# Kernel optimization log

Measured on AMD Instinct MI355X. Metric: run time of the kernel, lower is better.

## Reference

```python
import jax, jax.numpy as jnp
import numpy as np
import math

B, S, D_MODEL = 8, 1024, 1024
N_INPUT, N_PROCESS = 256, 512
N_HEADS, N_HEADS_IN = 8, 4
HIDDEN = 2 * N_INPUT  # combination_analyzer hidden dim (default n_input*2)
TEMP = 2.0            # router temperature buffer


def _mha(x, w_in, b_in, w_out, b_out, n_heads):
    """torch nn.MultiheadAttention (batch_first, eval mode) self-attention."""
    Bq, Sq, E = x.shape
    qkv = x @ w_in.T + b_in                      # [B,S,3E]
    q, k, v = jnp.split(qkv, 3, axis=-1)
    dh = E // n_heads
    sh = lambda t: t.reshape(Bq, Sq, n_heads, dh).transpose(0, 2, 1, 3)
    q, k, v = sh(q), sh(k), sh(v)
    scores = jnp.einsum('bhqd,bhkd->bhqk', q, k) * (1.0 / math.sqrt(dh))
    attn = jax.nn.softmax(scores, axis=-1)
    out = jnp.einsum('bhqk,bhkd->bhqd', attn, v).transpose(0, 2, 1, 3).reshape(Bq, Sq, E)
    return out @ w_out.T + b_out


def _ln(x, g, b, eps=1e-5):
    m = x.mean(-1, keepdims=True)
    v = ((x - m) ** 2).mean(-1, keepdims=True)
    return (x - m) / jnp.sqrt(v + eps) * g + b


def setup_inputs() -> dict:
    key = jax.random.key(0)
    ks = jax.random.split(key, 24)
    rn = lambda i, shape, s=0.02: jax.random.normal(ks[i], shape, jnp.float32) * s
    return {
        'x': jax.random.normal(ks[0], (B, S, D_MODEL), jnp.float32),
        # DynamicRouter attention (embed=d_model, heads=8)
        'r_in_w': rn(1, (3 * D_MODEL, D_MODEL)), 'r_in_b': jnp.zeros((3 * D_MODEL,), jnp.float32),
        'r_out_w': rn(2, (D_MODEL, D_MODEL)), 'r_out_b': jnp.zeros((D_MODEL,), jnp.float32),
        'aff_w': rn(3, (N_INPUT, D_MODEL)), 'aff_b': jnp.zeros((N_INPUT,), jnp.float32),
        # InputNeurons
        'patterns': rn(4, (N_INPUT, D_MODEL), 0.05),
        'i_in_w': rn(5, (3 * N_INPUT, N_INPUT)), 'i_in_b': jnp.zeros((3 * N_INPUT,), jnp.float32),
        'i_out_w': rn(6, (N_INPUT, N_INPUT)), 'i_out_b': jnp.zeros((N_INPUT,), jnp.float32),
        'ln_g': jnp.ones((N_INPUT,), jnp.float32), 'ln_b': jnp.zeros((N_INPUT,), jnp.float32),
        # ProcessNeurons
        'comb_w': rn(7, (N_PROCESS, N_INPUT), 0.05),
        'out_proj_w': rn(8, (N_PROCESS, D_MODEL), 0.05),
        'a1_w': rn(9, (HIDDEN, N_INPUT)), 'a1_b': jnp.zeros((HIDDEN,), jnp.float32),
        'a2_w': rn(10, (N_PROCESS, HIDDEN)), 'a2_b': jnp.zeros((N_PROCESS,), jnp.float32),
        'k_input': 128, 'k_process': 256,
    }


def reference(x, r_in_w, r_in_b, r_out_w, r_out_b, aff_w, aff_b, patterns,
              i_in_w, i_in_b, i_out_w, i_out_b, ln_g, ln_b,
              comb_w, out_proj_w, a1_w, a1_b, a2_w, a2_b, k_input, k_process):
    Bq = x.shape[0]
    # ---- DynamicRouter (eval mode: no gumbel noise, no score noise) ----
    context = _mha(x, r_in_w, r_in_b, r_out_w, r_out_b, N_HEADS)      # [B,S,D]
    affinity = context @ aff_w.T + aff_b                              # [B,S,N_INPUT]
    scores = affinity.max(axis=1)                                     # [B,N_INPUT]
    logits = scores / TEMP
    soft_w = jax.nn.softmax(logits, axis=-1)
    _, indices = jax.lax.top_k(logits, k_input)                       # [B,k_in]
    mask = jnp.zeros_like(soft_w).at[jnp.arange(Bq)[:, None], indices].set(1.0)
    masked = soft_w * mask
    weights = masked / (masked.sum(-1, keepdims=True) + 1e-8)         # [B,N_INPUT]
    # ---- InputNeurons (eval: dropout off) ----
    acts = jax.nn.gelu(context @ patterns.T, approximate=False)       # [B,S,N_INPUT]
    attn_out = _mha(acts, i_in_w, i_in_b, i_out_w, i_out_b, N_HEADS_IN)
    acts = _ln(acts + attn_out, ln_g, ln_b)
    # ---- Gather routed input neurons, weighted by routing weights ----
    sel_acts = jnp.take_along_axis(acts, indices[:, None, :], axis=2)  # [B,S,k_in]
    sel_w = jnp.take_along_axis(weights, indices, axis=1)              # [B,k_in]
    sel_acts = sel_acts * sel_w[:, None, :]
    # ---- ProcessNeurons ----
    # selected_weights[b,p,j] = comb_w[p, indices[b,j]]
    sel_cw = jnp.take(comb_w, indices, axis=1).transpose(1, 0, 2)      # [B,P,k_in]
    proc_acts = jax.nn.gelu(jnp.einsum('bsk,bpk->bsp', sel_acts, sel_cw), approximate=False)
    input_sel = jnp.zeros((Bq, N_INPUT), jnp.float32).at[jnp.arange(Bq)[:, None], indices].set(1.0)
    relevance = jax.nn.gelu(input_sel @ a1_w.T + a1_b, approximate=False) @ a2_w.T + a2_b  # [B,P]
    act_scores = proc_acts.max(axis=1)                                 # [B,P]
    final_scores = act_scores * jax.nn.sigmoid(relevance)
    _, pidx = jax.lax.top_k(final_scores, k_process)                   # [B,k_p]
    sel_proc = jnp.take_along_axis(proc_acts, pidx[:, None, :], axis=2)  # [B,S,k_p]
    sel_proj = out_proj_w[pidx]                                        # [B,k_p,D]
    out = jnp.einsum('bsk,bkd->bsd', sel_proc, sel_proj)               # [B,S,D]
    # ---- residual (eval: dropout identity) ----
    return x + out
```

## Files before the change

### kernel.cpp

```cpp
#include <hip/hip_runtime.h>
#include <hip/hip_bf16.h>
#include <math.h>

constexpr int NB = 8, NS = 1024, ND = 1024, NIN = 256, NPROC = 512, KIN = 128, KPROC = 256;

typedef __attribute__((ext_vector_type(8))) short bf16x8;
typedef __attribute__((ext_vector_type(4))) float f32x4;

#define VMCNT(n) asm volatile("s_waitcnt vmcnt(" #n ")" ::: "memory")
#define LGKMCNT(n) asm volatile("s_waitcnt lgkmcnt(" #n ")" ::: "memory")

__device__ inline float gelu_f(float x) {
    return 0.5f * x * (1.0f + erff(x * 0.7071067811865476f));
}
__device__ inline unsigned short f2b(float f) {
    __hip_bfloat16 h = __float2bfloat16(f);
    return *reinterpret_cast<unsigned short*>(&h);
}
__device__ inline void gload16(const void* g, void* l) {
    __builtin_amdgcn_global_load_lds(
        (const __attribute__((address_space(1))) void*)g,
        (__attribute__((address_space(3))) void*)l, 16, 0, 0);
}

__global__ __launch_bounds__(256)
void cvt_all_kernel(const float* __restrict__ x, const float* __restrict__ rin,
                    const float* __restrict__ rout, const float* __restrict__ affw,
                    const float* __restrict__ patt, const float* __restrict__ iin,
                    const float* __restrict__ iout, const float* __restrict__ aff_b,
                    unsigned short* __restrict__ xb, unsigned short* __restrict__ rinb,
                    unsigned short* __restrict__ routb, unsigned short* __restrict__ affbw,
                    unsigned short* __restrict__ pattb, unsigned short* __restrict__ iinb,
                    unsigned short* __restrict__ ioutb, float* __restrict__ biascat)
{
    if (blockIdx.x == 0) {
        int t = threadIdx.x;
        biascat[t] = aff_b[t];
        biascat[256 + t] = 0.f;
    }
    long gi = (long)blockIdx.x * 256 + threadIdx.x;
    long stride = (long)gridDim.x * 256;
    for (; gi < 3342336; gi += stride) {
        const float4* s; ushort4* d; long off;
        if (gi < 2097152)      { s = (const float4*)x;    d = (ushort4*)xb;    off = gi; }
        else if (gi < 2883584) { s = (const float4*)rin;  d = (ushort4*)rinb;  off = gi - 2097152; }
        else if (gi < 3145728) { s = (const float4*)rout; d = (ushort4*)routb; off = gi - 2883584; }
        else if (gi < 3211264) { s = (const float4*)affw; d = (ushort4*)affbw; off = gi - 3145728; }
        else if (gi < 3276800) { s = (const float4*)patt; d = (ushort4*)pattb; off = gi - 3211264; }
        else if (gi < 3325952) { s = (const float4*)iin;  d = (ushort4*)iinb;  off = gi - 3276800; }
        else                   { s = (const float4*)iout; d = (ushort4*)ioutb; off = gi - 3325952; }
        float4 v = s[off];
        ushort4 o;
        o.x = f2b(v.x); o.y = f2b(v.y); o.z = f2b(v.z); o.w = f2b(v.w);
        d[off] = o;
    }
}

__global__ __launch_bounds__(256)
void gemm128s(const unsigned short* __restrict__ A, int lda,
              const unsigned short* __restrict__ B, int ldb,
              const float* __restrict__ bias,
              unsigned short* __restrict__ C16, int ldc,
              int K, int nbx)
{
    __shared__ __align__(16) unsigned short Ab[3][128 * 32];
    __shared__ __align__(16) unsigned short Bb[3][128 * 32];
    int o = blockIdx.x;
    int cpx = gridDim.x >> 3;
    int swz = (o & 7) * cpx + (o >> 3);
    int by = swz / nbx, bx = swz - by * nbx;
    int row0 = by * 128, col0 = bx * 128;

    int t = threadIdx.x;
    int w = t >> 6, l = t & 63, l15 = l & 15, g = l >> 4;
    int wr = w >> 1, wc = w & 1;
    int NT = K >> 5;

    f32x4 acc[4][4];
#pragma unroll
    for (int i = 0; i < 4; ++i)
#pragma unroll
        for (int j = 0; j < 4; ++j) acc[i][j] = (f32x4){0.f, 0.f, 0.f, 0.f};

    auto STAGE = [&](int c, int kt) {
        int k0 = kt * 32;
#pragma unroll
        for (int i = 0; i < 2; ++i) {
            int gi = t + i * 256;
            int row = gi >> 2, cg = gi & 3;
            int cgs = cg ^ ((row >> 1) & 3);
            gload16(&A[(long)(row0 + row) * lda + k0 + cgs * 8], &Ab[c][gi * 8]);
        }
#pragma unroll
        for (int i = 0; i < 2; ++i) {
            int gi = t + i * 256;
            int row = gi >> 2, cg = gi & 3;
            int cgs = cg ^ ((row >> 1) & 3);
            gload16(&B[(long)(col0 + row) * ldb + k0 + cgs * 8], &Bb[c][gi * 8]);
        }
    };

    STAGE(0, 0);
    STAGE(1, 1);

    int cbr = (g ^ ((l15 >> 1) & 3)) * 16;

    int cur = 0;
    for (int T = 0; T < NT; ++T) {
        if (T + 1 < NT) { VMCNT(4); } else { VMCNT(0); }
        __builtin_amdgcn_s_barrier();
        asm volatile("" ::: "memory");

        const char* Ab_ = (const char*)&Ab[cur][0];
        const char* Bb_ = (const char*)&Bb[cur][0];
        bf16x8 af[4], bfr[4];
#pragma unroll
        for (int mi = 0; mi < 4; ++mi)
            af[mi] = *(const bf16x8*)(Ab_ + (wr * 64 + mi * 16 + l15) * 64 + cbr);
#pragma unroll
        for (int ni = 0; ni < 4; ++ni)
            bfr[ni] = *(const bf16x8*)(Bb_ + (wc * 64 + ni * 16 + l15) * 64 + cbr);

        if (T + 2 < NT) {
            int nxt = cur + 2;
            if (nxt >= 3) nxt -= 3;
            STAGE(nxt, T + 2);
        }

        LGKMCNT(0);
        __builtin_amdgcn_sched_barrier(0);
        __builtin_amdgcn_s_setprio(1);
#pragma unroll
        for (int mi = 0; mi < 4; ++mi)
#pragma unroll
            for (int ni = 0; ni < 4; ++ni)
                acc[mi][ni] = __builtin_amdgcn_mfma_f32_16x16x32_bf16(
                    af[mi], bfr[ni], acc[mi][ni], 0, 0, 0);
        __builtin_amdgcn_s_setprio(0);

        cur = (cur == 2) ? 0 : cur + 1;
    }

#pragma unroll
    for (int mi = 0; mi < 4; ++mi) {
#pragma unroll
        for (int ni = 0; ni < 4; ++ni) {
            int col = col0 + wc * 64 + ni * 16 + l15;
            float bv = bias ? bias[col] : 0.f;
#pragma unroll
            for (int r = 0; r < 4; ++r) {
                int row = row0 + wr * 64 + mi * 16 + g * 4 + r;
                float v = acc[mi][ni][r] + bv;
                float vp = __shfl_xor(v, 1);
                if (!(l15 & 1)) {
                    unsigned int u = (unsigned int)f2b(v) | ((unsigned int)f2b(vp) << 16);
                    *(unsigned int*)&C16[(long)row * ldc + col] = u;
                }
            }
        }
    }
}

__global__ __launch_bounds__(256)
void gemm128x64(const unsigned short* __restrict__ A, int lda,
                const unsigned short* __restrict__ B, int ldb,
                const float* __restrict__ bias,
                unsigned short* __restrict__ C16, int ldc,
                int K, int nbx)
{
    __shared__ __align__(16) unsigned short Ab[3][128 * 32];
    __shared__ __align__(16) unsigned short Bb[3][64 * 32];
    int o = blockIdx.x;
    int cpx = gridDim.x >> 3;
    int swz = (o & 7) * cpx + (o >> 3);
    int by = swz / nbx, bx = swz - by * nbx;
    int row0 = by * 128, col0 = bx * 64;

    int t = threadIdx.x;
    int w = t >> 6, l = t & 63, l15 = l & 15, g = l >> 4;
    int wr = w >> 1, wc = w & 1;
    int NT = K >> 5;

    f32x4 acc[4][2];
#pragma unroll
    for (int i = 0; i < 4; ++i)
#pragma unroll
        for (int j = 0; j < 2; ++j) acc[i][j] = (f32x4){0.f, 0.f, 0.f, 0.f};

    auto STAGE = [&](int c, int kt) {
        int k0 = kt * 32;
#pragma unroll
        for (int i = 0; i < 2; ++i) {
            int gi = t + i * 256;
            int row = gi >> 2, cg = gi & 3;
            int cgs = cg ^ ((row >> 1) & 3);
            gload16(&A[(long)(row0 + row) * lda + k0 + cgs * 8], &Ab[c][gi * 8]);
        }
        {
            int gi = t;
            int row = gi >> 2, cg = gi & 3;
            int cgs = cg ^ ((row >> 1) & 3);
            gload16(&B[(long)(col0 + row) * ldb + k0 + cgs * 8], &Bb[c][gi * 8]);
        }
    };

    STAGE(0, 0);
    STAGE(1, 1);

    int cbr = (g ^ ((l15 >> 1) & 3)) * 16;

    int cur = 0;
    for (int T = 0; T < NT; ++T) {
        if (T + 1 < NT) { VMCNT(3); } else { VMCNT(0); }
        __builtin_amdgcn_s_barrier();
        asm volatile("" ::: "memory");

        const char* Ab_ = (const char*)&Ab[cur][0];
        const char* Bb_ = (const char*)&Bb[cur][0];
        bf16x8 af[4], bfr[2];
#pragma unroll
        for (int mi = 0; mi < 4; ++mi)
            af[mi] = *(const bf16x8*)(Ab_ + (wr * 64 + mi * 16 + l15) * 64 + cbr);
#pragma unroll
        for (int ni = 0; ni < 2; ++ni)
            bfr[ni] = *(const bf16x8*)(Bb_ + (wc * 32 + ni * 16 + l15) * 64 + cbr);

        if (T + 2 < NT) {
            int nxt = cur + 2;
            if (nxt >= 3) nxt -= 3;
            STAGE(nxt, T + 2);
        }

        LGKMCNT(0);
        __builtin_amdgcn_sched_barrier(0);
        __builtin_amdgcn_s_setprio(1);
#pragma unroll
        for (int mi = 0; mi < 4; ++mi)
#pragma unroll
            for (int ni = 0; ni < 2; ++ni)
                acc[mi][ni] = __builtin_amdgcn_mfma_f32_16x16x32_bf16(
                    af[mi], bfr[ni], acc[mi][ni], 0, 0, 0);
        __builtin_amdgcn_s_setprio(0);

        cur = (cur == 2) ? 0 : cur + 1;
    }

#pragma unroll
    for (int mi = 0; mi < 4; ++mi) {
#pragma unroll
        for (int ni = 0; ni < 2; ++ni) {
            int col = col0 + wc * 32 + ni * 16 + l15;
            float bv = bias ? bias[col] : 0.f;
#pragma unroll
            for (int r = 0; r < 4; ++r) {
                int row = row0 + wr * 64 + mi * 16 + g * 4 + r;
                float v = acc[mi][ni][r] + bv;
                float vp = __shfl_xor(v, 1);
                if (!(l15 & 1)) {
                    unsigned int u = (unsigned int)f2b(v) | ((unsigned int)f2b(vp) << 16);
                    *(unsigned int*)&C16[(long)row * ldc + col] = u;
                }
            }
        }
    }
}

__global__ __launch_bounds__(256)
void gemm128e(const unsigned short* __restrict__ A, long sA, int lda,
              const unsigned short* __restrict__ B, long sB, int ldb,
              const float* __restrict__ bias,
              const float* __restrict__ resid, long sR, int ldr,
              float* __restrict__ C32, long sC32, int ldc32,
              unsigned short* __restrict__ C16, long sC16, int ldc16,
              float* __restrict__ C32b, int ldc32b,
              int K, int nbx, int act)
{
    __shared__ __align__(16) unsigned short Ab[3][128 * 32];
    __shared__ __align__(16) unsigned short Bb[3][64 * 32];
    int bz = blockIdx.z;
    const unsigned short* Abase = A + (long)bz * sA;
    const unsigned short* Bbase = B + (long)bz * sB;
    int o = blockIdx.x;
    int cpx = gridDim.x >> 3;
    int swz = (o & 7) * cpx + (o >> 3);
    int by = swz / nbx, bx = swz - by * nbx;
    int row0 = by * 128, col0 = bx * 64;

    int t = threadIdx.x;
    int w = t >> 6, l = t & 63, l15 = l & 15, g = l >> 4;
    int wr = w >> 1, wc = w & 1;
    int NT = K >> 5;

    f32x4 acc[4][2];
#pragma unroll
    for (int i = 0; i < 4; ++i)
#pragma unroll
        for (int j = 0; j < 2; ++j) acc[i][j] = (f32x4){0.f, 0.f, 0.f, 0.f};

    auto STAGE = [&](int c, int kt) {
        int k0 = kt * 32;
#pragma unroll
        for (int i = 0; i < 2; ++i) {
            int gi = t + i * 256;
            int row = gi >> 2, cg = gi & 3;
            int cgs = cg ^ ((row >> 1) & 3);
            gload16(&Abase[(long)(row0 + row) * lda + k0 + cgs * 8], &Ab[c][gi * 8]);
        }
        {
            int gi = t;
            int row = gi >> 2, cg = gi & 3;
            int cgs = cg ^ ((row >> 1) & 3);
            gload16(&Bbase[(long)(col0 + row) * ldb + k0 + cgs * 8], &Bb[c][gi * 8]);
        }
    };

    STAGE(0, 0);
    STAGE(1, 1);

    int cbr = (g ^ ((l15 >> 1) & 3)) * 16;

    int cur = 0;
    for (int T = 0; T < NT; ++T) {
        if (T + 1 < NT) { VMCNT(3); } else { VMCNT(0); }
        __builtin_amdgcn_s_barrier();
        asm volatile("" ::: "memory");

        const char* Ab_ = (const char*)&Ab[cur][0];
        const char* Bb_ = (const char*)&Bb[cur][0];
        bf16x8 af[4], bfr[2];
#pragma unroll
        for (int mi = 0; mi < 4; ++mi)
            af[mi] = *(const bf16x8*)(Ab_ + (wr * 64 + mi * 16 + l15) * 64 + cbr);
#pragma unroll
        for (int ni = 0; ni < 2; ++ni)
            bfr[ni] = *(const bf16x8*)(Bb_ + (wc * 32 + ni * 16 + l15) * 64 + cbr);

        if (T + 2 < NT) {
            int nxt = cur + 2;
            if (nxt >= 3) nxt -= 3;
            STAGE(nxt, T + 2);
        }

        LGKMCNT(0);
        __builtin_amdgcn_sched_barrier(0);
        __builtin_amdgcn_s_setprio(1);
#pragma unroll
        for (int mi = 0; mi < 4; ++mi)
#pragma unroll
            for (int ni = 0; ni < 2; ++ni)
                acc[mi][ni] = __builtin_amdgcn_mfma_f32_16x16x32_bf16(
                    af[mi], bfr[ni], acc[mi][ni], 0, 0, 0);
        __builtin_amdgcn_s_setprio(0);

        cur = (cur == 2) ? 0 : cur + 1;
    }

#pragma unroll
    for (int mi = 0; mi < 4; ++mi) {
#pragma unroll
        for (int ni = 0; ni < 2; ++ni) {
            int col = col0 + wc * 32 + ni * 16 + l15;
            float bv = bias ? bias[col] : 0.f;
#pragma unroll
            for (int r = 0; r < 4; ++r) {
                int row = row0 + wr * 64 + mi * 16 + g * 4 + r;
                float v = acc[mi][ni][r] + bv;
                if (act == 2) {
                    if (col < 256) {
                        C32[(long)row * ldc32 + col] = v;
                    } else {
                        v = gelu_f(v);
                        C32b[(long)row * ldc32b + (col - 256)] = v;
                        C16[(long)row * ldc16 + (col - 256)] = f2b(v);
                    }
                    continue;
                }
                if (act == 1) v = gelu_f(v);
                if (resid) v += resid[(long)bz * sR + (long)row * ldr + col];
                if (C32) C32[(long)bz * sC32 + (long)row * ldc32 + col] = v;
                if (C16) C16[(long)bz * sC16 + (long)row * ldc16 + col] = f2b(v);
            }
        }
    }
}

template <int D>
__global__ __launch_bounds__(256, 2)
void attn_mfma(unsigned short* __restrict__ qkv, int stride, int koff, int voff, float scale)
{
    constexpr int GRL = D / 8;
    constexpr int NITK = (64 * GRL) / 256;
    constexpr int NITV = NITK;
    constexpr int NKS = D / 32;
    constexpr int NF = D / 16;
    constexpr int LV = 72;
    constexpr int LP = 72;
    constexpr int NT = NS / 64;

    __shared__ __align__(16) unsigned short Ks[2][64 * D];
    __shared__ __align__(16) unsigned short Vt[D * LV];
    __shared__ __align__(16) unsigned short Ps[128 * LP];

    int b = blockIdx.z, h = blockIdx.y, qt = blockIdx.x;
    int t = threadIdx.x, w = t >> 6, l = t & 63, l15 = l & 15, g = l >> 4;
    int wq = w * 32;
    long qbase = ((long)b * NS + qt * 128) * stride + h * D;
    long kvbase = (long)b * NS * stride + h * D;

    bf16x8 qreg[2][NKS];
#pragma unroll
    for (int qh = 0; qh < 2; ++qh)
#pragma unroll
        for (int ks = 0; ks < NKS; ++ks)
            qreg[qh][ks] = *(const bf16x8*)&qkv[qbase + (long)(wq + qh * 16 + l15) * stride + g * 8 + ks * 32];

    auto KSTAGE = [&](int c, int kt) {
#pragma unroll
        for (int i = 0; i < NITK; ++i) {
            int gi = t + i * 256;
            int row = gi / GRL, cg = gi % GRL;
            int cgs = cg ^ (row & 7);
            gload16(&qkv[kvbase + (long)(kt * 64 + row) * stride + koff + cgs * 8],
                    &Ks[c][gi * 8]);
        }
    };
    uint4 vp[NITV];
    auto VLOAD = [&](int kt) {
#pragma unroll
        for (int i = 0; i < NITV; ++i) {
            int vgi = t + i * 256;
            int kc = vgi & 63, db = vgi >> 6;
            vp[i] = *(const uint4*)&qkv[kvbase + (long)(kt * 64 + kc) * stride + voff + db * 8];
        }
    };
    auto VWRITE = [&]() {
#pragma unroll
        for (int i = 0; i < NITV; ++i) {
            int vgi = t + i * 256;
            int kc = vgi & 63, db = vgi >> 6;
            uint4 v = vp[i];
            Vt[(db * 8 + 0) * LV + kc] = (unsigned short)(v.x & 0xffff);
            Vt[(db * 8 + 1) * LV + kc] = (unsigned short)(v.x >> 16);
            Vt[(db * 8 + 2) * LV + kc] = (unsigned short)(v.y & 0xffff);
            Vt[(db * 8 + 3) * LV + kc] = (unsigned short)(v.y >> 16);
            Vt[(db * 8 + 4) * LV + kc] = (unsigned short)(v.z & 0xffff);
            Vt[(db * 8 + 5) * LV + kc] = (unsigned short)(v.z >> 16);
            Vt[(db * 8 + 6) * LV + kc] = (unsigned short)(v.w & 0xffff);
            Vt[(db * 8 + 7) * LV + kc] = (unsigned short)(v.w >> 16);
        }
    };

    KSTAGE(0, 0);
    VLOAD(0);
    KSTAGE(1, 1);
    if constexpr (NITK == 4) { VMCNT(4); } else { VMCNT(2); }
    VWRITE();
    LGKMCNT(0);
    __builtin_amdgcn_sched_barrier(0);
    __builtin_amdgcn_s_barrier();

    float m_run[2] = {-INFINITY, -INFINITY};
    float l_run[2] = {0.f, 0.f};
    f32x4 zero4 = {0.f, 0.f, 0.f, 0.f};
    f32x4 oacc[2][NF];
#pragma unroll
    for (int qh = 0; qh < 2; ++qh)
#pragma unroll
        for (int nf = 0; nf < NF; ++nf) oacc[qh][nf] = zero4;

    int xr = (l15 & 7) << 4;
    for (int kt = 0; kt < NT; ++kt) {
        if (kt + 1 < NT) VLOAD(kt + 1);

        const char* ksb = (const char*)&Ks[kt & 1][0];
        f32x4 st[4][2];
#pragma unroll
        for (int f = 0; f < 4; ++f)
#pragma unroll
            for (int qh = 0; qh < 2; ++qh) st[f][qh] = zero4;
#pragma unroll
        for (int ks = 0; ks < NKS; ++ks) {
#pragma unroll
            for (int f = 0; f < 4; ++f) {
                int cb = (g * 16 + ks * 64) ^ xr;
                bf16x8 a = *(const bf16x8*)(ksb + (f * 16 + l15) * (D * 2) + cb);
#pragma unroll
                for (int qh = 0; qh < 2; ++qh)
                    st[f][qh] = __builtin_amdgcn_mfma_f32_16x16x32_bf16(a, qreg[qh][ks], st[f][qh], 0, 0, 0);
            }
        }
#pragma unroll
        for (int qh = 0; qh < 2; ++qh) {
            float pm = -INFINITY;
#pragma unroll
            for (int f = 0; f < 4; ++f) {
                st[f][qh] *= scale;
#pragma unroll
                for (int r = 0; r < 4; ++r) pm = fmaxf(pm, st[f][qh][r]);
            }
            pm = fmaxf(pm, __shfl_xor(pm, 16));
            pm = fmaxf(pm, __shfl_xor(pm, 32));
            float mn = fmaxf(m_run[qh], pm);
            float corr = __expf(m_run[qh] - mn);
            float rs = 0.f;
#pragma unroll
            for (int f = 0; f < 4; ++f) {
                float p0 = __expf(st[f][qh][0] - mn);
                float p1 = __expf(st[f][qh][1] - mn);
                float p2 = __expf(st[f][qh][2] - mn);
                float p3 = __expf(st[f][qh][3] - mn);
                rs += (p0 + p1) + (p2 + p3);
                ushort4 pw;
                pw.x = f2b(p0); pw.y = f2b(p1); pw.z = f2b(p2); pw.w = f2b(p3);
                *(ushort4*)&Ps[(wq + qh * 16 + l15) * LP + f * 16 + g * 4] = pw;
            }
            rs += __shfl_xor(rs, 16);
            rs += __shfl_xor(rs, 32);
            l_run[qh] = l_run[qh] * corr + rs;
            m_run[qh] = mn;
            float corrO[4];
#pragma unroll
            for (int r = 0; r < 4; ++r) corrO[r] = __shfl(corr, g * 4 + r);
#pragma unroll
            for (int nf = 0; nf < NF; ++nf)
#pragma unroll
                for (int r = 0; r < 4; ++r) oacc[qh][nf][r] *= corrO[r];
        }
#pragma unroll
        for (int ks2 = 0; ks2 < 2; ++ks2) {
            bf16x8 vb[NF];
#pragma unroll
            for (int nf = 0; nf < NF; ++nf)
                vb[nf] = *(const bf16x8*)&Vt[(nf * 16 + l15) * LV + ks2 * 32 + g * 8];
#pragma unroll
            for (int qh = 0; qh < 2; ++qh) {
                bf16x8 pa = *(const bf16x8*)&Ps[(wq + qh * 16 + l15) * LP + ks2 * 32 + g * 8];
#pragma unroll
                for (int nf = 0; nf < NF; ++nf)
                    oacc[qh][nf] = __builtin_amdgcn_mfma_f32_16x16x32_bf16(pa, vb[nf], oacc[qh][nf], 0, 0, 0);
            }
        }

        if (kt + 1 < NT) {
            LGKMCNT(0);
            __builtin_amdgcn_sched_barrier(0);
            __builtin_amdgcn_s_barrier();
            if (kt + 2 < NT) {
                KSTAGE(kt & 1, kt + 2);
                if constexpr (NITK == 4) { VMCNT(4); } else { VMCNT(2); }
            } else {
                VMCNT(0);
            }
            VWRITE();
            LGKMCNT(0);
            __builtin_amdgcn_sched_barrier(0);
            __builtin_amdgcn_s_barrier();
        }
    }

#pragma unroll
    for (int qh = 0; qh < 2; ++qh) {
        float lo[4];
#pragma unroll
        for (int r = 0; r < 4; ++r) lo[r] = __shfl(l_run[qh], g * 4 + r);
#pragma unroll
        for (int nf = 0; nf < NF; ++nf)
#pragma unroll
            for (int r = 0; r < 4; ++r) {
                float o = oacc[qh][nf][r] / lo[r];
                qkv[qbase + (long)(wq + qh * 16 + g * 4 + r) * stride + nf * 16 + l15] = f2b(o);
            }
    }
}

__global__ __launch_bounds__(256)
void maxpart_aff_kernel(const float* __restrict__ aff, float* __restrict__ part)
{
    int sc = blockIdx.x, b = blockIdx.y, t = threadIdx.x;
    float m = -INFINITY;
    for (int s = sc * 32; s < (sc + 1) * 32; ++s)
        m = fmaxf(m, aff[((long)b * NS + s) * NIN + t]);
    part[(b * 32 + sc) * NIN + t] = m;
}

__global__ __launch_bounds__(256)
void rank_input_kernel(const float* __restrict__ part, int* __restrict__ idx_out,
                       float* __restrict__ w_out)
{
    int b = blockIdx.x, t = threadIdx.x;
    __shared__ float lg[256], rv[256];
    float m = part[(b * 32) * NIN + t];
#pragma unroll
    for (int sc = 1; sc < 32; ++sc) m = fmaxf(m, part[(b * 32 + sc) * NIN + t]);
    float l = m * 0.5f;
    lg[t] = l;
    rv[t] = l;
    __syncthreads();
    for (int off = 128; off; off >>= 1) {
        if (t < off) rv[t] = fmaxf(rv[t], rv[t + off]);
        __syncthreads();
    }
    float mx = rv[0];
    __syncthreads();
    float e = expf(l - mx);
    rv[t] = e;
    __syncthreads();
    for (int off = 128; off; off >>= 1) {
        if (t < off) rv[t] += rv[t + off];
        __syncthreads();
    }
    float Zs = rv[0];
    float soft = e / Zs;
    __syncthreads();
    int rank = 0;
    for (int j = 0; j < 256; ++j) {
        float vj = lg[j];
        rank += (vj > l) || (vj == l && j < t);
    }
    rv[t] = (rank < KIN) ? soft : 0.f;
    __syncthreads();
    for (int off = 128; off; off >>= 1) {
        if (t < off) rv[t] += rv[t + off];
        __syncthreads();
    }
    float msum = rv[0];
    if (rank < KIN) {
        idx_out[b * KIN + rank] = t;
        w_out[b * KIN + rank] = soft / (msum + 1e-8f);
    }
}

__global__ __launch_bounds__(512)
void rank_proc_kernel(const float* __restrict__ finals, int* __restrict__ pidx)
{
    int b = blockIdx.x, t = threadIdx.x;
    __shared__ float v[512];
    float xv = finals[b * NPROC + t];
    v[t] = xv;
    __syncthreads();
    int rank = 0;
    for (int j = 0; j < 512; ++j) {
        float vj = v[j];
        rank += (vj > xv) || (vj == xv && j < t);
    }
    if (rank < KPROC) pidx[b * KPROC + rank] = t;
}

__global__ __launch_bounds__(256)
void ln_gather_kernel(const float* __restrict__ a, const float* __restrict__ bsrc,
                      const float* __restrict__ gg, const float* __restrict__ be,
                      const int* __restrict__ idx_in, const float* __restrict__ w_sel,
                      unsigned short* __restrict__ sel_acts)
{
    long row = blockIdx.x;
    int b = blockIdx.x >> 10;
    int t = threadIdx.x;
    float v = a[row * 256 + t] + bsrc[row * 256 + t];
    __shared__ float rv[256];
    __shared__ float lnv[256];
    rv[t] = v;
    __syncthreads();
    for (int off = 128; off; off >>= 1) {
        if (t < off) rv[t] += rv[t + off];
        __syncthreads();
    }
    float mean = rv[0] * (1.f / 256.f);
    __syncthreads();
    float d = v - mean;
    rv[t] = d * d;
    __syncthreads();
    for (int off = 128; off; off >>= 1) {
        if (t < off) rv[t] += rv[t + off];
        __syncthreads();
    }
    float var = rv[0] * (1.f / 256.f);
    lnv[t] = d * rsqrtf(var + 1e-5f) * gg[t] + be[t];
    __syncthreads();
    if (t < KIN) {
        int id = idx_in[b * KIN + t];
        sel_acts[row * KIN + t] = f2b(lnv[id] * w_sel[b * KIN + t]);
    }
}

__global__ void gather_sel_cw_b(const float* __restrict__ comb_w, const int* __restrict__ idx_in,
                                unsigned short* __restrict__ sel_cw)
{
    int gidx = blockIdx.x * 256 + threadIdx.x;
    int b = gidx >> 16;
    int rem = gidx & 65535;
    int pb = rem >> 7, j = rem & 127;
    sel_cw[gidx] = f2b(comb_w[pb * NIN + idx_in[b * KIN + j]]);
}

__global__ void gather_sel_proc_b(const float* __restrict__ proc_acts, const int* __restrict__ pidx,
                                  unsigned short* __restrict__ sel_proc)
{
    int s = blockIdx.x, b = blockIdx.y, j = threadIdx.x;
    long row = (long)b * NS + s;
    sel_proc[row * KPROC + j] = f2b(proc_acts[row * NPROC + pidx[b * KPROC + j]]);
}

__global__ void gather_sel_projT(const float* __restrict__ out_proj_w, const int* __restrict__ pidx,
                                 unsigned short* __restrict__ selT)
{
    int gidx = blockIdx.x * 256 + threadIdx.x;
    int b = gidx >> 15;
    int rem = gidx & 32767;
    int d = rem >> 5;
    int kp0 = (rem & 31) * 8;
    unsigned int u[4];
#pragma unroll
    for (int i = 0; i < 4; ++i) {
        unsigned short e0 = f2b(out_proj_w[(long)pidx[b * KPROC + kp0 + 2 * i] * ND + d]);
        unsigned short e1 = f2b(out_proj_w[(long)pidx[b * KPROC + kp0 + 2 * i + 1] * ND + d]);
        u[i] = (unsigned int)e0 | ((unsigned int)e1 << 16);
    }
    uint4 o; o.x = u[0]; o.y = u[1]; o.z = u[2]; o.w = u[3];
    *(uint4*)&selT[((long)b * ND + d) * KPROC + kp0] = o;
}

__global__ __launch_bounds__(512)
void maxpart_kernel(const float* __restrict__ proc, float* __restrict__ part)
{
    int sc = blockIdx.x, b = blockIdx.y, t = threadIdx.x;
    float m = -INFINITY;
    for (int s = sc * 32; s < (sc + 1) * 32; ++s)
        m = fmaxf(m, proc[((long)b * NS + s) * NPROC + t]);
    part[(b * 32 + sc) * NPROC + t] = m;
}

__global__ __launch_bounds__(512)
void relevance_kernel(const float* __restrict__ part, const int* __restrict__ idx_in,
                      const float* __restrict__ a1w, const float* __restrict__ a1b,
                      const float* __restrict__ a2w, const float* __restrict__ a2b,
                      float* __restrict__ finals)
{
    int b = blockIdx.x, t = threadIdx.x;
    float m = part[(b * 32) * NPROC + t];
#pragma unroll
    for (int sc = 1; sc < 32; ++sc) m = fmaxf(m, part[(b * 32 + sc) * NPROC + t]);
    __shared__ float rel1[512];
    __shared__ int sidx[KIN];
    if (t < KIN) sidx[t] = idx_in[b * KIN + t];
    __syncthreads();
    float r1 = a1b[t];
    const float* a1row = a1w + (long)t * NIN;
    for (int j = 0; j < KIN; ++j) r1 += a1row[sidx[j]];
    rel1[t] = gelu_f(r1);
    __syncthreads();
    float r = a2b[t];
    const float* a2row = a2w + (long)t * 512;
    for (int hh = 0; hh < 512; ++hh) r += rel1[hh] * a2row[hh];
    float sig = 1.f / (1.f + expf(-r));
    finals[b * NPROC + t] = m * sig;
}

extern "C" void kernel_launch(void* const* d_in, const int* in_sizes, int n_in,
                              void* d_out, int out_size, void* d_ws, size_t ws_size,
                              hipStream_t stream)
{
    const float* x       = (const float*)d_in[0];
    const float* r_in_w  = (const float*)d_in[1];
    const float* r_in_b  = (const float*)d_in[2];
    const float* r_out_w = (const float*)d_in[3];
    const float* r_out_b = (const float*)d_in[4];
    const float* aff_w   = (const float*)d_in[5];
    const float* aff_b   = (const float*)d_in[6];
    const float* patterns= (const float*)d_in[7];
    const float* i_in_w  = (const float*)d_in[8];
    const float* i_in_b  = (const float*)d_in[9];
    const float* i_out_w = (const float*)d_in[10];
    const float* i_out_b = (const float*)d_in[11];
    const float* ln_g    = (const float*)d_in[12];
    const float* ln_b    = (const float*)d_in[13];
    const float* comb_w  = (const float*)d_in[14];
    const float* out_proj_w = (const float*)d_in[15];
    const float* a1w     = (const float*)d_in[16];
    const float* a1b     = (const float*)d_in[17];
    const float* a2w     = (const float*)d_in[18];
    const float* a2b     = (const float*)d_in[19];
    float* out = (float*)d_out;

    char* ws = (char*)d_ws;
    unsigned short* qkv1b    = (unsigned short*)(ws + 0);
    unsigned short* contextb = (unsigned short*)(ws + 50331648);
    unsigned short* xb       = (unsigned short*)(ws + 67108864);
    unsigned short* w_rin_b  = (unsigned short*)(ws + 83886080);
    unsigned short* w_rout_b = (unsigned short*)(ws + 90177536);
    unsigned short* w_aff_b  = (unsigned short*)(ws + 92274688);
    unsigned short* patt_b   = (unsigned short*)(ws + 92798976);
    unsigned short* w_iin_b  = (unsigned short*)(ws + 93323264);
    unsigned short* w_iout_b = (unsigned short*)(ws + 93716480);
    float* w_sel   = (float*)(ws + 93855744);
    int*   idx_in  = (int*)(ws + 93859840);
    float* finals  = (float*)(ws + 93863936);
    int*   pidx    = (int*)(ws + 93880320);
    float* affin   = (float*)(ws + 94019584);
    float* acts0   = (float*)(ws + 102408192);
    unsigned short* acts0b = (unsigned short*)(ws + 110796800);
    unsigned short* qkv2b  = (unsigned short*)(ws + 114991104);
    float* attn2proj = (float*)(ws + 0);
    float* proc_acts = (float*)(ws + 16777216);
    unsigned short* sel_actsb = (unsigned short*)(ws + 33554432);
    unsigned short* sel_cwb   = (unsigned short*)(ws + 35651584);
    unsigned short* sel_procb = (unsigned short*)(ws + 36700160);
    unsigned short* sel_projT = (unsigned short*)(ws + 40894464);
    float* biascat  = (float*)(ws + 45088768);
    float* part_aff = (float*)(ws + 45091840);
    float* maxpart  = (float*)(ws + 45353984);

    cvt_all_kernel<<<2048, 256, 0, stream>>>(
        x, r_in_w, r_out_w, aff_w, patterns, i_in_w, i_out_w, aff_b,
        xb, w_rin_b, w_rout_b, w_aff_b, patt_b, w_iin_b, w_iout_b, biascat);

    gemm128s<<<1536, 256, 0, stream>>>(xb, ND, w_rin_b, ND, r_in_b, qkv1b, 3 * ND, ND, 24);
    attn_mfma<128><<<dim3(8, 8, 8), 256, 0, stream>>>(qkv1b, 3 * ND, ND, 2 * ND, 0.088388347648318447f);
    gemm128x64<<<1024, 256, 0, stream>>>(qkv1b, 3 * ND, w_rout_b, ND, r_out_b, contextb, ND, ND, 16);
    gemm128e<<<dim3(512, 1, 1), 256, 0, stream>>>(
        contextb, 0, ND, w_aff_b, 0, ND, biascat, nullptr, 0, 0,
        affin, 0, NIN, acts0b, 0, NIN, acts0, NIN, ND, 8, 2);
    maxpart_aff_kernel<<<dim3(32, NB), 256, 0, stream>>>(affin, part_aff);
    rank_input_kernel<<<NB, 256, 0, stream>>>(part_aff, idx_in, w_sel);
    gemm128x64<<<768, 256, 0, stream>>>(acts0b, NIN, w_iin_b, NIN, i_in_b, qkv2b, 3 * NIN, NIN, 12);
    attn_mfma<64><<<dim3(8, 4, 8), 256, 0, stream>>>(qkv2b, 3 * NIN, NIN, 2 * NIN, 0.125f);
    gemm128e<<<dim3(256, 1, 1), 256, 0, stream>>>(
        qkv2b, 0, 3 * NIN, w_iout_b, 0, NIN, i_out_b, nullptr, 0, 0,
        attn2proj, 0, NIN, nullptr, 0, 0, nullptr, 0, NIN, 4, 0);
    ln_gather_kernel<<<NB * NS, 256, 0, stream>>>(acts0, attn2proj, ln_g, ln_b,
                                                  idx_in, w_sel, sel_actsb);
    gather_sel_cw_b<<<2048, 256, 0, stream>>>(comb_w, idx_in, sel_cwb);
    gemm128e<<<dim3(64, 1, NB), 256, 0, stream>>>(
        sel_actsb, (long)NS * KIN, KIN, sel_cwb, (long)NPROC * KIN, KIN,
        nullptr, nullptr, 0, 0,
        proc_acts, (long)NS * NPROC, NPROC, nullptr, 0, 0, nullptr, 0, KIN, 8, 1);
    maxpart_kernel<<<dim3(32, NB), 512, 0, stream>>>(proc_acts, maxpart);
    relevance_kernel<<<NB, 512, 0, stream>>>(maxpart, idx_in, a1w, a1b, a2w, a2b, finals);
    rank_proc_kernel<<<NB, 512, 0, stream>>>(finals, pidx);
    gather_sel_proc_b<<<dim3(NS, NB), KPROC, 0, stream>>>(proc_acts, pidx, sel_procb);
    gather_sel_projT<<<1024, 256, 0, stream>>>(out_proj_w, pidx, sel_projT);
    gemm128e<<<dim3(128, 1, NB), 256, 0, stream>>>(
        sel_procb, (long)NS * KPROC, KPROC, sel_projT, (long)ND * KPROC, KPROC,
        nullptr, x, (long)NS * ND, ND,
        out, (long)NS * ND, ND, nullptr, 0, 0, nullptr, 0, KPROC, 16, 0);
    (void)in_sizes; (void)n_in; (void)out_size; (void)ws_size;
}
```

Measured before the change: 427.8 us.

## Store intermediate activations in bf16, wave-level layernorm, split relevance into parallel kernels

After: 406.4 us (median of 3 runs). -5.0%, faster.

```diff
diff --git a/kernel.cpp b/kernel.cpp
--- a/kernel.cpp
+++ b/kernel.cpp
@@ -16,6 +16,10 @@
 __device__ inline unsigned short f2b(float f) {
     __hip_bfloat16 h = __float2bfloat16(f);
     return *reinterpret_cast<unsigned short*>(&h);
+}
+__device__ inline float b2f(unsigned short u) {
+    unsigned int v = (unsigned int)u << 16;
+    return __uint_as_float(v);
 }
 __device__ inline void gload16(const void* g, void* l) {
     __builtin_amdgcn_global_load_lds(
@@ -647,39 +651,41 @@
 }
 
 __global__ __launch_bounds__(256)
-void ln_gather_kernel(const float* __restrict__ a, const float* __restrict__ bsrc,
+void ln_gather_kernel(const float* __restrict__ a, const unsigned short* __restrict__ bsrc,
                       const float* __restrict__ gg, const float* __restrict__ be,
                       const int* __restrict__ idx_in, const float* __restrict__ w_sel,
                       unsigned short* __restrict__ sel_acts)
 {
-    long row = blockIdx.x;
-    int b = blockIdx.x >> 10;
-    int t = threadIdx.x;
-    float v = a[row * 256 + t] + bsrc[row * 256 + t];
-    __shared__ float rv[256];
-    __shared__ float lnv[256];
-    rv[t] = v;
-    __syncthreads();
-    for (int off = 128; off; off >>= 1) {
-        if (t < off) rv[t] += rv[t + off];
-        __syncthreads();
-    }
-    float mean = rv[0] * (1.f / 256.f);
-    __syncthreads();
-    float d = v - mean;
-    rv[t] = d * d;
-    __syncthreads();
-    for (int off = 128; off; off >>= 1) {
-        if (t < off) rv[t] += rv[t + off];
-        __syncthreads();
-    }
-    float var = rv[0] * (1.f / 256.f);
-    lnv[t] = d * rsqrtf(var + 1e-5f) * gg[t] + be[t];
-    __syncthreads();
-    if (t < KIN) {
-        int id = idx_in[b * KIN + t];
-        sel_acts[row * KIN + t] = f2b(lnv[id] * w_sel[b * KIN + t]);
-    }
+    int w = threadIdx.x >> 6, l = threadIdx.x & 63;
+    long row = (long)blockIdx.x * 4 + w;
+    int b = (int)(row >> 10);
+    __shared__ float lnv[4][256];
+
+    float4 av = *(const float4*)&a[row * 256 + l * 4];
+    ushort4 bu = *(const ushort4*)&bsrc[row * 256 + l * 4];
+    float v0 = av.x + b2f(bu.x);
+    float v1 = av.y + b2f(bu.y);
+    float v2 = av.z + b2f(bu.z);
+    float v3 = av.w + b2f(bu.w);
+    float s = (v0 + v1) + (v2 + v3);
+#pragma unroll
+    for (int off = 1; off < 64; off <<= 1) s += __shfl_xor(s, off);
+    float mean = s * (1.f / 256.f);
+    float d0 = v0 - mean, d1 = v1 - mean, d2 = v2 - mean, d3 = v3 - mean;
+    float ss = (d0 * d0 + d1 * d1) + (d2 * d2 + d3 * d3);
+#pragma unroll
+    for (int off = 1; off < 64; off <<= 1) ss += __shfl_xor(ss, off);
+    float rstd = rsqrtf(ss * (1.f / 256.f) + 1e-5f);
+    float4 gv = *(const float4*)&gg[l * 4];
+    float4 bev = *(const float4*)&be[l * 4];
+    lnv[w][l * 4 + 0] = d0 * rstd * gv.x + bev.x;
+    lnv[w][l * 4 + 1] = d1 * rstd * gv.y + bev.y;
+    lnv[w][l * 4 + 2] = d2 * rstd * gv.z + bev.z;
+    lnv[w][l * 4 + 3] = d3 * rstd * gv.w + bev.w;
+    int id0 = idx_in[b * KIN + l];
+    int id1 = idx_in[b * KIN + l + 64];
+    sel_acts[row * KIN + l] = f2b(lnv[w][id0] * w_sel[b * KIN + l]);
+    sel_acts[row * KIN + l + 64] = f2b(lnv[w][id1] * w_sel[b * KIN + l + 64]);
 }
 
 __global__ void gather_sel_cw_b(const float* __restrict__ comb_w, const int* __restrict__ idx_in,
@@ -692,12 +698,13 @@
     sel_cw[gidx] = f2b(comb_w[pb * NIN + idx_in[b * KIN + j]]);
 }
 
-__global__ void gather_sel_proc_b(const float* __restrict__ proc_acts, const int* __restrict__ pidx,
+__global__ void gather_sel_proc_b(const unsigned short* __restrict__ proc_acts,
+                                  const int* __restrict__ pidx,
                                   unsigned short* __restrict__ sel_proc)
 {
     int s = blockIdx.x, b = blockIdx.y, j = threadIdx.x;
     long row = (long)b * NS + s;
-    sel_proc[row * KPROC + j] = f2b(proc_acts[row * NPROC + pidx[b * KPROC + j]]);
+    sel_proc[row * KPROC + j] = proc_acts[row * NPROC + pidx[b * KPROC + j]];
 }
 
 __global__ void gather_sel_projT(const float* __restrict__ out_proj_w, const int* __restrict__ pidx,
@@ -720,39 +727,58 @@
 }
 
 __global__ __launch_bounds__(512)
-void maxpart_kernel(const float* __restrict__ proc, float* __restrict__ part)
+void maxpart_kernel(const unsigned short* __restrict__ proc, float* __restrict__ part)
 {
     int sc = blockIdx.x, b = blockIdx.y, t = threadIdx.x;
     float m = -INFINITY;
     for (int s = sc * 32; s < (sc + 1) * 32; ++s)
-        m = fmaxf(m, proc[((long)b * NS + s) * NPROC + t]);
+        m = fmaxf(m, b2f(proc[((long)b * NS + s) * NPROC + t]));
     part[(b * 32 + sc) * NPROC + t] = m;
 }
 
 __global__ __launch_bounds__(512)
-void relevance_kernel(const float* __restrict__ part, const int* __restrict__ idx_in,
-                      const float* __restrict__ a1w, const float* __restrict__ a1b,
-                      const float* __restrict__ a2w, const float* __restrict__ a2b,
-                      float* __restrict__ finals)
+void rel1_kernel(const int* __restrict__ idx_in, const float* __restrict__ a1w,
+                 const float* __restrict__ a1b, float* __restrict__ rel1g)
 {
     int b = blockIdx.x, t = threadIdx.x;
-    float m = part[(b * 32) * NPROC + t];
-#pragma unroll
-    for (int sc = 1; sc < 32; ++sc) m = fmaxf(m, part[(b * 32 + sc) * NPROC + t]);
-    __shared__ float rel1[512];
     __shared__ int sidx[KIN];
     if (t < KIN) sidx[t] = idx_in[b * KIN + t];
     __syncthreads();
     float r1 = a1b[t];
     const float* a1row = a1w + (long)t * NIN;
     for (int j = 0; j < KIN; ++j) r1 += a1row[sidx[j]];
-    rel1[t] = gelu_f(r1);
+    rel1g[b * 512 + t] = gelu_f(r1);
+}
+
+__global__ __launch_bounds__(256)
+void finals_kernel(const float* __restrict__ maxpart, const float* __restrict__ rel1g,
+                   const float* __restrict__ a2w, const float* __restrict__ a2b,
+                   float* __restrict__ finals)
+{
+    int b = blockIdx.y;
+    int w = threadIdx.x >> 6, l = threadIdx.x & 63;
+    __shared__ float r1[512];
+    for (int i = threadIdx.x; i < 512; i += 256) r1[i] = rel1g[b * 512 + i];
     __syncthreads();
-    float r = a2b[t];
-    const float* a2row = a2w + (long)t * 512;
-    for (int hh = 0; hh < 512; ++hh) r += rel1[hh] * a2row[hh];
-    float sig = 1.f / (1.f + expf(-r));
-    finals[b * NPROC + t] = m * sig;
+#pragma unroll 1
+    for (int pi = 0; pi < 16; ++pi) {
+        int p = blockIdx.x * 64 + w * 16 + pi;
+        const float* a2row = a2w + (long)p * 512;
+        float acc = 0.f;
+#pragma unroll
+        for (int i = 0; i < 8; ++i)
+            acc += a2row[l + i * 64] * r1[l + i * 64];
+#pragma unroll
+        for (int off = 1; off < 64; off <<= 1) acc += __shfl_xor(acc, off);
+        float m = (l < 32) ? maxpart[((long)b * 32 + l) * NPROC + p] : -INFINITY;
+#pragma unroll
+        for (int off = 1; off < 32; off <<= 1) m = fmaxf(m, __shfl_xor(m, off));
+        if (l == 0) {
+            float r = acc + a2b[p];
+            float sig = 1.f / (1.f + expf(-r));
+            finals[b * NPROC + p] = m * sig;
+        }
+    }
 }
 
 extern "C" void kernel_launch(void* const* d_in, const int* in_sizes, int n_in,
@@ -799,8 +825,8 @@
     float* acts0   = (float*)(ws + 102408192);
     unsigned short* acts0b = (unsigned short*)(ws + 110796800);
     unsigned short* qkv2b  = (unsigned short*)(ws + 114991104);
-    float* attn2proj = (float*)(ws + 0);
-    float* proc_acts = (float*)(ws + 16777216);
+    unsigned short* attn2projb = (unsigned short*)(ws + 0);
+    unsigned short* proc_actsb = (unsigned short*)(ws + 16777216);
     unsigned short* sel_actsb = (unsigned short*)(ws + 33554432);
     unsigned short* sel_cwb   = (unsigned short*)(ws + 35651584);
     unsigned short* sel_procb = (unsigned short*)(ws + 36700160);
@@ -808,6 +834,7 @@
     float* biascat  = (float*)(ws + 45088768);
     float* part_aff = (float*)(ws + 45091840);
     float* maxpart  = (float*)(ws + 45353984);
+    float* rel1g    = (float*)(ws + 45878272);
 
     cvt_all_kernel<<<2048, 256, 0, stream>>>(
         x, r_in_w, r_out_w, aff_w, patterns, i_in_w, i_out_w, aff_b,
@@ -825,18 +852,19 @@
     attn_mfma<64><<<dim3(8, 4, 8), 256, 0, stream>>>(qkv2b, 3 * NIN, NIN, 2 * NIN, 0.125f);
     gemm128e<<<dim3(256, 1, 1), 256, 0, stream>>>(
         qkv2b, 0, 3 * NIN, w_iout_b, 0, NIN, i_out_b, nullptr, 0, 0,
-        attn2proj, 0, NIN, nullptr, 0, 0, nullptr, 0, NIN, 4, 0);
-    ln_gather_kernel<<<NB * NS, 256, 0, stream>>>(acts0, attn2proj, ln_g, ln_b,
-                                                  idx_in, w_sel, sel_actsb);
+        nullptr, 0, 0, attn2projb, 0, NIN, nullptr, 0, NIN, 4, 0);
+    ln_gather_kernel<<<2048, 256, 0, stream>>>(acts0, attn2projb, ln_g, ln_b,
+                                               idx_in, w_sel, sel_actsb);
     gather_sel_cw_b<<<2048, 256, 0, stream>>>(comb_w, idx_in, sel_cwb);
     gemm128e<<<dim3(64, 1, NB), 256, 0, stream>>>(
         sel_actsb, (long)NS * KIN, KIN, sel_cwb, (long)NPROC * KIN, KIN,
         nullptr, nullptr, 0, 0,
-        proc_acts, (long)NS * NPROC, NPROC, nullptr, 0, 0, nullptr, 0, KIN, 8, 1);
-    maxpart_kernel<<<dim3(32, NB), 512, 0, stream>>>(proc_acts, maxpart);
-    relevance_kernel<<<NB, 512, 0, stream>>>(maxpart, idx_in, a1w, a1b, a2w, a2b, finals);
+        nullptr, 0, 0, proc_actsb, (long)NS * NPROC, NPROC, nullptr, 0, KIN, 8, 1);
+    maxpart_kernel<<<dim3(32, NB), 512, 0, stream>>>(proc_actsb, maxpart);
+    rel1_kernel<<<NB, 512, 0, stream>>>(idx_in, a1w, a1b, rel1g);
+    finals_kernel<<<dim3(8, NB), 256, 0, stream>>>(maxpart, rel1g, a2w, a2b, finals);
     rank_proc_kernel<<<NB, 512, 0, stream>>>(finals, pidx);
-    gather_sel_proc_b<<<dim3(NS, NB), KPROC, 0, stream>>>(proc_acts, pidx, sel_procb);
+    gather_sel_proc_b<<<dim3(NS, NB), KPROC, 0, stream>>>(proc_actsb, pidx, sel_procb);
     gather_sel_projT<<<1024, 256, 0, stream>>>(out_proj_w, pidx, sel_projT);
     gemm128e<<<dim3(128, 1, NB), 256, 0, stream>>>(
         sel_procb, (long)NS * KPROC, KPROC, sel_projT, (long)ND * KPROC, KPROC,
```
